# Kernel optimization log

Measured on AMD Instinct MI355X. Metric: run time of the kernel, lower is better.

## Reference

```python
import jax, jax.numpy as jnp
from jax import lax
import numpy as np

EVAL_TERMS = 10   # eval mode: num_terms = eval_terms, update_iters = 0
INIT_ITERS = 50   # power iterations done in __init__
KSIZE = 3
IDX = np.array([0, 1, 1, 2, 3, 4, 2, 4, 3])  # maps 5 coeffs -> 3x3 kernel
EPS = 1e-12


def _l2n(t, axis):
    return t / (jnp.sqrt(jnp.sum(t * t, axis=axis, keepdims=True)) + EPS)


def setup_inputs() -> dict:
    key = jax.random.key(0)
    kx, kw, kb, ku, kv = jax.random.split(key, 5)
    C = 64
    stdv = 1.0 / np.sqrt(C)
    return {
        "x": jax.random.normal(kx, (16, C, 192, 192), dtype=jnp.float32),
        "random_conv_filter": jax.random.normal(kw, (C, C, 5), dtype=jnp.float32) * stdv,
        "bias": jax.random.uniform(kb, (C,), dtype=jnp.float32, minval=-stdv, maxval=stdv),
        "u0": jax.random.normal(ku, (5, 1, C), dtype=jnp.float32),
        "v0": jax.random.normal(kv, (5, C, 1), dtype=jnp.float32),
    }


def _power_iter(A, u0, v0):
    # A: (num, C, C) (stop-gradient), u: (num,1,C), v: (num,C,1)
    u = _l2n(u0, 2)
    v = _l2n(v0, 1)
    def body(i, uv):
        u, v = uv
        v = _l2n(jnp.sum(A * u, axis=2, keepdims=True), 1)
        u = _l2n(jnp.sum(A * v, axis=1, keepdims=True), 2)
        return (u, v)
    return lax.fori_loop(0, INIT_ITERS, body, (u, v))


def reference(x, random_conv_filter, bias, u0, v0):
    C = random_conv_filter.shape[0]
    # skew-symmetric filter per coefficient slice: A = 0.5*(W - W^T)
    A = 0.5 * (random_conv_filter - jnp.transpose(random_conv_filter, (1, 0, 2)))
    A = jnp.transpose(A, (2, 0, 1))  # (num, C, C)
    # spectral norm via power iteration (buffers; no grad)
    u, v = _power_iter(lax.stop_gradient(A), u0, v0)
    u = lax.stop_gradient(u)
    v = lax.stop_gradient(v)
    sigmas = jnp.sum(A * v * u, axis=(1, 2))  # (num,), grad flows through A only
    An = A / sigmas[:, None, None]
    # Taylor series of expm: I + An + An^2/2! + ... (eval_terms=10)
    curr = An
    Fm = An
    for i in range(2, EVAL_TERMS + 1):
        curr = jnp.einsum('nij,njk->nik', curr, An) / float(i)
        Fm = Fm + curr
    Fm = Fm + jnp.eye(C, dtype=Fm.dtype)[None]
    Fm = jnp.transpose(Fm, (1, 2, 0))  # (C, C, num)
    # expand 5 coeffs to 3x3 kernel, then spatial ifft2 -> real
    K = Fm[:, :, IDX].reshape(C, C, KSIZE, KSIZE)
    K = jnp.fft.ifft2(K, axes=(-2, -1)).real.astype(x.dtype)
    w = x.shape[2]
    pad = w // KSIZE  # circular pad and matching dilation
    xp = jnp.pad(x, ((0, 0), (0, 0), (pad, pad), (pad, pad)), mode='wrap')
    z = lax.conv_general_dilated(
        xp, K, window_strides=(1, 1), padding='VALID',
        rhs_dilation=(pad, pad),
        dimension_numbers=('NCHW', 'OIHW', 'NCHW'))
    return z + bias[None, :, None, None]
```

## Files before the change

### kernel.cpp

```cpp
#include <hip/hip_runtime.h>

typedef __attribute__((ext_vector_type(8))) short short8;
typedef __attribute__((ext_vector_type(4))) float f32x4;
typedef __attribute__((ext_vector_type(4))) float float4v;
typedef __attribute__((ext_vector_type(4))) unsigned int u32x4;

__device__ __forceinline__ unsigned short f2bf(float f) {
    unsigned int u = __float_as_uint(f);
    u += 0x7fffu + ((u >> 16) & 1u);
    return (unsigned short)(u >> 16);
}

__device__ __forceinline__ float wavesum(float x) {
#pragma unroll
    for (int m = 1; m < 64; m <<= 1) x += __shfl_xor(x, m);
    return x;
}

__device__ __forceinline__ float wavemax(float x) {
#pragma unroll
    for (int m = 1; m < 64; m <<= 1) x = fmaxf(x, __shfl_xor(x, m));
    return x;
}

__device__ __forceinline__ float matvec64(const float* row, float y) {
    float ac[8] = {0.f, 0.f, 0.f, 0.f, 0.f, 0.f, 0.f, 0.f};
#pragma unroll
    for (int j = 0; j < 64; ++j) {
        const float yj =
            __uint_as_float(__builtin_amdgcn_readlane(__float_as_uint(y), j));
        ac[j & 7] = fmaf(row[j], yj, ac[j & 7]);
    }
    return ((ac[0] + ac[1]) + (ac[2] + ac[3])) + ((ac[4] + ac[5]) + (ac[6] + ac[7]));
}

__device__ __forceinline__ void gload16(const void* g, void* l) {
    __builtin_amdgcn_global_load_lds(
        (const __attribute__((address_space(1))) unsigned int*)g,
        (__attribute__((address_space(3))) unsigned int*)l, 16, 0, 0);
}

#define WTF_OFF       81920
#define WTOLD_OFF     745472
#define XT_OFF        1441792
#define WS_NEEDED     76939264UL

#define FM_AFP   0
#define FM_R0    17408
#define FM_R1    34816
#define FM_SLOT  52224
#define FM_RED   76800
#define FM_SMEM  76928

__device__ __forceinline__ void fm_matmul_sb(char* sm, int srcOff, int bfSrcSlot,
                                             int dstOff, int bfDstSlot, int t) {
    const float* src = (const float*)(sm + srcOff);
    const unsigned short* bfS =
        (const unsigned short*)(sm + FM_SLOT) + bfSrcSlot * 4096;
    float* dst = (float*)(sm + dstOff);
    float* redf = (float*)(sm + FM_RED);
    const int lane = t & 63;
    const int wv = t >> 6;
    const int lm = lane & 15, lg = lane >> 4;
    f32x4 acc[4] = {};
    if (t < 256) {
#pragma unroll
        for (int kk = 0; kk < 2; ++kk) {
            const float* ap = src + (16 * wv + lm) * 68 + kk * 32 + lg * 8;
            const f32x4 a0 = *(const f32x4*)ap;
            const f32x4 a1 = *(const f32x4*)(ap + 4);
            short8 ah;
#pragma unroll
            for (int j = 0; j < 4; ++j) {
                ah[j] = (short)f2bf(a0[j]);
                ah[j + 4] = (short)f2bf(a1[j]);
            }
#pragma unroll
            for (int cf = 0; cf < 4; ++cf) {
                const short8 b =
                    *(const short8*)(bfS + ((kk * 4 + cf) * 64 + lane) * 8);
                acc[cf] = __builtin_amdgcn_mfma_f32_16x16x32_bf16(ah, b, acc[cf],
                                                                  0, 0, 0);
            }
        }
        float mx = 0.0f;
#pragma unroll
        for (int cf = 0; cf < 4; ++cf)
#pragma unroll
            for (int r = 0; r < 4; ++r) mx = fmaxf(mx, fabsf(acc[cf][r]));
        mx = wavemax(mx);
        if (lane == 0) redf[wv] = mx;
    }
    __syncthreads();
    if (t < 256) {
        const float g = fmaxf(fmaxf(redf[0], redf[1]), fmaxf(redf[2], redf[3]));
        const float sc = 1.0f / g;
        unsigned short* bfD = (unsigned short*)(sm + FM_SLOT) + bfDstSlot * 4096;
#pragma unroll
        for (int cf = 0; cf < 4; ++cf) {
#pragma unroll
            for (int r = 0; r < 4; ++r) {
                const int k = 16 * wv + 4 * lg + r;
                const int nn = 16 * cf + lm;
                const float v = acc[cf][r] * sc;
                dst[k * 68 + nn] = v;
                if (bfDstSlot >= 0)
                    bfD[(((k >> 5) * 4 + cf) * 64 + ((k & 31) >> 3) * 16 + lm) * 8 +
                        (k & 7)] = f2bf(v);
            }
        }
    }
    __syncthreads();
}

__global__ __launch_bounds__(512) void fmconv_kernel(const float* __restrict__ W,
                                                     const float* __restrict__ u0,
                                                     const float* __restrict__ x,
                                                     float* __restrict__ FmOut,
                                                     unsigned short* __restrict__ xT) {
    __shared__ __align__(16) char smem[FM_SMEM];
    const int t = threadIdx.x;

    if (blockIdx.x >= 5) {
        float (*L0)[66] = (float (*)[66])smem;
        float (*L1)[66] = (float (*)[66])(smem + 8448);
        const int bb = blockIdx.x - 5;
        const int n = bb / 96;
        const int hpair = bb % 96;
        const int c = t >> 4;
        const int w4 = (t & 15) * 4;
        const int w2 = t >> 3;
        const int c4 = (t & 7) * 4;

#define XADDR(I)                                                                \
    (x + ((size_t)((n * 64 + ((I) & 1) * 32 + c) * 192 +                        \
                   (hpair * 2 + (I) / 6))) * 192 + (((I) >> 1) % 3) * 64 + w4)

        float4v r = *(const float4v*)XADDR(0);
        float4v rn;
#pragma unroll
        for (int i = 0; i < 12; ++i) {
            float (*L)[66] = (i & 1) ? L1 : L0;
            if (i < 11) rn = *(const float4v*)XADDR(i + 1);
            L[c][w4 + 0] = r[0];
            L[c][w4 + 1] = r[1];
            L[c][w4 + 2] = r[2];
            L[c][w4 + 3] = r[3];
            __syncthreads();
            union { unsigned short u[4]; unsigned long long q; } pk;
#pragma unroll
            for (int k = 0; k < 4; ++k) pk.u[k] = f2bf(L[c4 + k][w2]);
            const int half = i & 1;
            const int wb = (i >> 1) % 3;
            const int dh = i / 6;
            const size_t tilebase =
                ((size_t)(((n * 192 + hpair * 2 + dh) * 2 + half))) * 6144 + wb * 2048;
            *(unsigned long long*)(xT + tilebase + w2 * 32 + c4) = pk.q;
            r = rn;
        }
#undef XADDR
        return;
    }

    float* Afp = (float*)(smem + FM_AFP);
    float* R0f = (float*)(smem + FM_R0);
    float* R1f = (float*)(smem + FM_R1);
    float* redf = (float*)(smem + FM_RED);
    float* sigP = redf + 4;
    const int n = blockIdx.x;
    const int lane = t & 63;
    const int wv = t >> 6;
    const int lm = lane & 15, lg = lane >> 4;

    {
        const int i = t >> 3;
        const int j0 = (t & 7) * 8;
#pragma unroll
        for (int k = 0; k < 8; ++k) {
            const int j = j0 + k;
            const float wij = W[(i * 64 + j) * 5 + n];
            const float wji = W[(j * 64 + i) * 5 + n];
            Afp[i * 68 + j] = 0.5f * (wij - wji);
        }
    }
    __syncthreads();

    if (t < 256) {
        unsigned short* s0 = (unsigned short*)(smem + FM_SLOT);
#pragma unroll
        for (int cf = 0; cf < 4; ++cf) {
#pragma unroll
            for (int r = 0; r < 4; ++r) {
                const int k = 16 * wv + 4 * lg + r;
                const int nn = 16 * cf + lm;
                s0[(((k >> 5) * 4 + cf) * 64 + ((k & 31) >> 3) * 16 + lm) * 8 +
                   (k & 7)] = f2bf(Afp[k * 68 + nn]);
            }
        }
    }
    __syncthreads();

    fm_matmul_sb(smem, FM_AFP, 0, FM_R0, 1, t);
    fm_matmul_sb(smem, FM_R0, 1, FM_R1, 2, t);
    fm_matmul_sb(smem, FM_R1, 2, FM_R0, 0, t);
    fm_matmul_sb(smem, FM_R0, 0, FM_R1, 2, t);
    fm_matmul_sb(smem, FM_R1, 2, FM_R0, 0, t);
    fm_matmul_sb(smem, FM_R0, 0, FM_R1, -1, t);
    fm_matmul_sb(smem, FM_R1, 0, FM_R0, -1, t);
    fm_matmul_sb(smem, FM_R0, 1, FM_R1, -1, t);

    if (t < 64) {
        float row[64];
#pragma unroll
        for (int q = 0; q < 16; ++q)
            *(f32x4*)&row[q * 4] = *(const f32x4*)&R1f[t * 68 + q * 4];
        float u = u0[n * 64 + t];
        u = u / (sqrtf(wavesum(u * u)) + 1e-12f);
        const float w = matvec64(row, u);
#pragma unroll
        for (int q = 0; q < 16; ++q)
            *(f32x4*)&row[q * 4] = *(const f32x4*)&Afp[t * 68 + q * 4];
        const float tt = matvec64(row, w);
        const float v = tt / (sqrtf(wavesum(tt * tt)) + 1e-12f);
        const float s = matvec64(row, v);
        const float u50 = -s / (sqrtf(wavesum(s * s)) + 1e-12f);
        const float t2 = matvec64(row, u50);
        const float sig = wavesum(v * t2);
        if (t == 0) *sigP = sig;
    }
    __syncthreads();

    const float inv_sig = 1.0f / (*sigP);
    float Fm[4][4];
    if (t < 256) {
        unsigned int* Anpk = (unsigned int*)(smem + FM_SLOT);
#pragma unroll
        for (int cf = 0; cf < 4; ++cf) {
#pragma unroll
            for (int r = 0; r < 4; ++r) {
                const int k = 16 * wv + 4 * lg + r;
                const int nn = 16 * cf + lm;
                const float v = Afp[k * 68 + nn] * inv_sig;
                R0f[k * 68 + nn] = v;
                const unsigned int ph = f2bf(v);
                const float hf = __uint_as_float(ph << 16);
                const unsigned int pl = f2bf(v - hf);
                Anpk[(((k >> 5) * 4 + cf) * 64 + ((k & 31) >> 3) * 16 + lm) * 8 +
                     (k & 7)] = ph | (pl << 16);
                Fm[cf][r] = v;
            }
        }
    }
    __syncthreads();

    for (int term = 2; term <= 10; ++term) {
        f32x4 acc[4] = {};
        if (t < 256) {
            const unsigned int* Anpk = (const unsigned int*)(smem + FM_SLOT);
#pragma unroll
            for (int kk = 0; kk < 2; ++kk) {
                const float* ap = R0f + (16 * wv + lm) * 68 + kk * 32 + lg * 8;
                const f32x4 a0 = *(const f32x4*)ap;
                const f32x4 a1 = *(const f32x4*)(ap + 4);
                short8 ah, al;
#pragma unroll
                for (int j = 0; j < 4; ++j) {
                    const unsigned int h0 = f2bf(a0[j]);
                    ah[j] = (short)h0;
                    al[j] = (short)f2bf(a0[j] - __uint_as_float(h0 << 16));
                    const unsigned int h1 = f2bf(a1[j]);
                    ah[j + 4] = (short)h1;
                    al[j + 4] = (short)f2bf(a1[j] - __uint_as_float(h1 << 16));
                }
#pragma unroll
                for (int cf = 0; cf < 4; ++cf) {
                    const unsigned int* pp = Anpk + ((kk * 4 + cf) * 64 + lane) * 8;
                    const u32x4 p0 = *(const u32x4*)pp;
                    const u32x4 p1 = *(const u32x4*)(pp + 4);
                    short8 bh, bl;
#pragma unroll
                    for (int j = 0; j < 4; ++j) {
                        bh[j] = (short)(p0[j] & 0xffffu);
                        bl[j] = (short)(p0[j] >> 16);
                        bh[j + 4] = (short)(p1[j] & 0xffffu);
                        bl[j + 4] = (short)(p1[j] >> 16);
                    }
                    acc[cf] = __builtin_amdgcn_mfma_f32_16x16x32_bf16(ah, bh,
                                                                      acc[cf], 0, 0, 0);
                    acc[cf] = __builtin_amdgcn_mfma_f32_16x16x32_bf16(ah, bl,
                                                                      acc[cf], 0, 0, 0);
                    acc[cf] = __builtin_amdgcn_mfma_f32_16x16x32_bf16(al, bh,
                                                                      acc[cf], 0, 0, 0);
                }
            }
        }
        __syncthreads();
        if (t < 256) {
            const float sc = 1.0f / (float)term;
#pragma unroll
            for (int cf = 0; cf < 4; ++cf) {
#pragma unroll
                for (int r = 0; r < 4; ++r) {
                    const int k = 16 * wv + 4 * lg + r;
                    const int nn = 16 * cf + lm;
                    const float v = acc[cf][r] * sc;
                    Fm[cf][r] += v;
                    if (term < 10) R0f[k * 68 + nn] = v;
                }
            }
        }
        __syncthreads();
    }

    if (t < 256) {
#pragma unroll
        for (int cf = 0; cf < 4; ++cf) {
#pragma unroll
            for (int r = 0; r < 4; ++r) {
                const int k = 16 * wv + 4 * lg + r;
                const int nn = 16 * cf + lm;
                FmOut[n * 4096 + k * 64 + nn] = Fm[cf][r] + ((k == nn) ? 1.0f : 0.0f);
            }
        }
    }
}

__global__ __launch_bounds__(256) void wbuild_kernel(const float* __restrict__ Fm,
                                                     unsigned short* __restrict__ Wtf,
                                                     unsigned short* __restrict__ WtOld) {
    const int tg = blockIdx.x * 256 + threadIdx.x;
    const int o = tg >> 6;
    const int i = tg & 63;
    float f[5];
#pragma unroll
    for (int nn = 0; nn < 5; ++nn) f[nn] = Fm[nn * 4096 + o * 64 + i];
    const int idx[3][3] = {{0, 1, 1}, {2, 3, 4}, {2, 4, 3}};
    float Kk[3][3];
#pragma unroll
    for (int u = 0; u < 3; ++u) {
#pragma unroll
        for (int v = 0; v < 3; ++v) {
            float s = 0.0f;
#pragma unroll
            for (int p = 0; p < 3; ++p) {
#pragma unroll
                for (int q = 0; q < 3; ++q) {
                    const int m = (p * u + q * v) % 3;
                    s += f[idx[p][q]] * ((m == 0) ? 1.0f : -0.5f);
                }
            }
            Kk[u][v] = s * (1.0f / 9.0f);
        }
    }
#pragma unroll
    for (int a = 0; a < 3; ++a) {
#pragma unroll
        for (int b = 0; b < 3; ++b) {
            const int m = (a * 3 + b) * 64 + o;
#pragma unroll
            for (int al = 0; al < 3; ++al) {
#pragma unroll
                for (int be = 0; be < 3; ++be) {
                    const int kh = (al - a + 4) % 3;
                    const int kw = (be - b + 4) % 3;
                    const unsigned short bf = f2bf(Kk[kh][kw]);
                    const int kap = (al * 3 + be) * 64 + i;
                    WtOld[m * 576 + kap] = bf;
                    const int MF = m >> 4, lmx = m & 15;
                    const int cc = kap >> 5, lgx = (kap >> 3) & 3, j = kap & 7;
                    Wtf[MF * 9216 + cc * 512 + (lgx * 16 + lmx) * 8 + j] = bf;
                }
            }
        }
    }
}

__global__ __launch_bounds__(256, 2) void gemm4_kernel(
    const unsigned short* __restrict__ xT, const unsigned short* __restrict__ Wtf,
    const float* __restrict__ bias, float* __restrict__ out) {
    __shared__ __align__(16) char smem[81920];
    const int t = threadIdx.x;
    const int lane = t & 63;
    const int wv = t >> 6;
    const int wm = wv >> 1;
    const int wp = wv & 1;
    const int lm = lane & 15;
    const int lg = lane >> 4;

    const int orig = blockIdx.x;
    const int swz = (orig & 7) * 192 + (orig >> 3);
    const int mg = swz % 3;
    const int panel = swz / 3;
    const int n = panel >> 5;
    const int h0b = (panel & 31) * 2;

    f32x4 acc[6][4] = {};

#define STAGE(BUF, KC)                                                          \
    {                                                                           \
        const int al_ = (KC) / 3, be_ = (KC) - 3 * ((KC) / 3);                  \
        _Pragma("unroll") for (int it = 0; it < 10; ++it) {                     \
            char* ldsb = smem + (BUF) * 40960 + it * 4096 + wv * 1024;          \
            const unsigned short* src;                                          \
            if (it < 6) {                                                       \
                const int e = it * 2048 + t * 8;                                \
                const int mfL = e >> 10;                                        \
                const int rem = e & 1023;                                       \
                src = Wtf + (mg * 12 + mfL) * 9216 + (KC) * 1024 + rem;         \
            } else {                                                            \
                const int e = (it - 6) * 2048 + t * 8;                          \
                const int ccL = e >> 12;                                        \
                const int rem = e & 4095;                                       \
                const int p_ = rem >> 5;                                        \
                const int c_ = rem & 31;                                        \
                const int h_ = h0b + (p_ >> 6) + 64 * al_;                      \
                const int w_ = be_ * 64 + (p_ & 63);                            \
                src = xT + ((size_t)((n * 192 + h_) * 2 + ccL)) * 6144 +        \
                      w_ * 32 + c_;                                             \
            }                                                                   \
            gload16(src, ldsb);                                                 \
        }                                                                       \
    }

#define COMPUTE(BUF)                                                            \
    {                                                                           \
        const char* base = smem + (BUF) * 40960;                                \
        short8 af[12];                                                          \
        short8 bf[8];                                                           \
        _Pragma("unroll") for (int mf = 0; mf < 6; ++mf)                        \
            _Pragma("unroll") for (int cl = 0; cl < 2; ++cl)                    \
                af[mf * 2 + cl] = *(const short8*)(                             \
                    base + (wm * 6 + mf) * 2048 + cl * 1024 + lane * 16);       \
        _Pragma("unroll") for (int pf = 0; pf < 4; ++pf)                        \
            _Pragma("unroll") for (int cl = 0; cl < 2; ++cl)                    \
                bf[pf * 2 + cl] = *(const short8*)(                             \
                    base + 24576 + cl * 8192 +                                  \
                    (wp * 64 + pf * 16 + lm) * 64 + lg * 16);                   \
        _Pragma("unroll") for (int cl = 0; cl < 2; ++cl)                        \
            _Pragma("unroll") for (int mf = 0; mf < 6; ++mf)                    \
                _Pragma("unroll") for (int pf = 0; pf < 4; ++pf)                \
                    acc[mf][pf] = __builtin_amdgcn_mfma_f32_16x16x32_bf16(      \
                        af[mf * 2 + cl], bf[pf * 2 + cl], acc[mf][pf], 0, 0, 0);\
    }

    STAGE(0, 0);
    __syncthreads();
#pragma unroll
    for (int kc = 0; kc < 9; ++kc) {
        const int b = kc & 1;
        if (kc < 8) STAGE(b ^ 1, kc + 1);
        COMPUTE(b);
        if (kc < 8) __syncthreads();
    }
#undef STAGE
#undef COMPUTE

    const int h0 = h0b + wp;
#pragma unroll
    for (int mf = 0; mf < 6; ++mf) {
#pragma unroll
        for (int r = 0; r < 4; ++r) {
            const int m = mg * 192 + wm * 96 + mf * 16 + lg * 4 + r;
            const int o = m & 63;
            const int ab2 = m >> 6;
            const float bo = bias[o];
            const int rowoff =
                ((n * 64 + o) * 192 + (h0 + 64 * (ab2 / 3))) * 192 + 64 * (ab2 % 3);
#pragma unroll
            for (int pf = 0; pf < 4; ++pf) {
                out[rowoff + pf * 16 + lm] = acc[mf][pf][r] + bo;
            }
        }
    }
}

__global__ __launch_bounds__(256) void gemm_fallback(const float* __restrict__ x,
                                                     const unsigned short* __restrict__ Wt,
                                                     const float* __restrict__ bias,
                                                     float* __restrict__ out) {
    __shared__ unsigned short Xs[64][36];
    const int t = threadIdx.x;
    const int lane = t & 63;
    const int wv = t >> 6;
    const int pblk = blockIdx.x;
    const int mg = blockIdx.y;
    const int n = pblk >> 6;
    const int h0 = pblk & 63;
    const int wave_m0 = mg * 192 + wv * 48;
    const int lm = lane & 15;
    const int lg = lane >> 4;

    f32x4 acc[3][4] = {};
    const float* xb = x + n * 64 * 36864;
    const int w0s = t & 63;
    const int kq = (t >> 6) * 8;

    for (int c = 0; c < 18; ++c) {
        const int ab = c >> 1;
        const int al = ab / 3;
        const int be = ab % 3;
        const int ih = (c & 1) * 32;
        const int base = ih * 36864 + (h0 + 64 * al) * 192 + 64 * be + w0s;
#pragma unroll
        for (int s = 0; s < 8; ++s) {
            const int kp = kq + s;
            Xs[w0s][kp] = f2bf(xb[base + kp * 36864]);
        }
        __syncthreads();
        const int kb = c * 32 + lg * 8;
        short8 af[3];
#pragma unroll
        for (int mf = 0; mf < 3; ++mf)
            af[mf] = *(const short8*)(Wt + (wave_m0 + mf * 16 + lm) * 576 + kb);
        short8 bf[4];
#pragma unroll
        for (int pf = 0; pf < 4; ++pf) {
            union { short8 v; unsigned long long q[2]; } u;
            const unsigned long long* s8 =
                (const unsigned long long*)(&Xs[pf * 16 + lm][lg * 8]);
            u.q[0] = s8[0];
            u.q[1] = s8[1];
            bf[pf] = u.v;
        }
#pragma unroll
        for (int mf = 0; mf < 3; ++mf)
#pragma unroll
            for (int pf = 0; pf < 4; ++pf)
                acc[mf][pf] = __builtin_amdgcn_mfma_f32_16x16x32_bf16(
                    af[mf], bf[pf], acc[mf][pf], 0, 0, 0);
        __syncthreads();
    }

#pragma unroll
    for (int mf = 0; mf < 3; ++mf)
#pragma unroll
        for (int r = 0; r < 4; ++r) {
            const int m = wave_m0 + mf * 16 + lg * 4 + r;
            const int o = m & 63;
            const int ab2 = m >> 6;
            const float bo = bias[o];
            const int rowoff =
                ((n * 64 + o) * 192 + (h0 + 64 * (ab2 / 3))) * 192 + 64 * (ab2 % 3);
#pragma unroll
            for (int pf = 0; pf < 4; ++pf)
                out[rowoff + pf * 16 + lm] = acc[mf][pf][r] + bo;
        }
}

extern "C" void kernel_launch(void* const* d_in, const int* in_sizes, int n_in,
                              void* d_out, int out_size, void* d_ws, size_t ws_size,
                              hipStream_t stream) {
    (void)in_sizes; (void)n_in; (void)out_size;
    const float* x = (const float*)d_in[0];
    const float* W = (const float*)d_in[1];
    const float* bias = (const float*)d_in[2];
    const float* u0 = (const float*)d_in[3];
    float* out = (float*)d_out;

    float* Fm = (float*)d_ws;
    unsigned short* Wtf = (unsigned short*)((char*)d_ws + WTF_OFF);
    unsigned short* WtOld = (unsigned short*)((char*)d_ws + WTOLD_OFF);
    unsigned short* xT = (unsigned short*)((char*)d_ws + XT_OFF);

    const bool big_ws = (ws_size >= WS_NEEDED);

    if (big_ws) {
        fmconv_kernel<<<5 + 1536, 512, 0, stream>>>(W, u0, x, Fm, xT);
        wbuild_kernel<<<16, 256, 0, stream>>>(Fm, Wtf, WtOld);
        gemm4_kernel<<<1536, 256, 0, stream>>>(xT, Wtf, bias, out);
    } else {
        fmconv_kernel<<<5, 512, 0, stream>>>(W, u0, x, Fm, xT);
        wbuild_kernel<<<16, 256, 0, stream>>>(Fm, Wtf, WtOld);
        dim3 g(1024, 3, 1);
        gemm_fallback<<<g, 256, 0, stream>>>(x, WtOld, bias, out);
    }
}
```

Baseline: 112.8 us.

## Fuse x bf16 conversion into GEMM B-tile staging, drop xT pre-pass

Removes the separate pass that transposed x into a bf16 xT workspace buffer. The GEMM kernel now loads fp32 x into registers, converts it to bf16 and writes the B tile to LDS itself, with register prefetch overlapping the MFMA compute. This saves the extra global write and re-read of the intermediate tensor. In exchange the GEMM carries more registers, and its uncoalesced fp32 loads (stride across channels) plus the LDS stores sit on its critical path.

```diff
diff --git a/kernel.cpp b/kernel.cpp
--- a/kernel.cpp
+++ b/kernel.cpp
@@ -42,8 +42,7 @@
 
 #define WTF_OFF       81920
 #define WTOLD_OFF     745472
-#define XT_OFF        1441792
-#define WS_NEEDED     76939264UL
+#define WS_NEEDED     1409024UL
 
 #define FM_AFP   0
 #define FM_R0    17408
@@ -113,55 +112,11 @@
     __syncthreads();
 }
 
-__global__ __launch_bounds__(512) void fmconv_kernel(const float* __restrict__ W,
-                                                     const float* __restrict__ u0,
-                                                     const float* __restrict__ x,
-                                                     float* __restrict__ FmOut,
-                                                     unsigned short* __restrict__ xT) {
+__global__ __launch_bounds__(512) void fm_kernel(const float* __restrict__ W,
+                                                 const float* __restrict__ u0,
+                                                 float* __restrict__ FmOut) {
     __shared__ __align__(16) char smem[FM_SMEM];
     const int t = threadIdx.x;
-
-    if (blockIdx.x >= 5) {
-        float (*L0)[66] = (float (*)[66])smem;
-        float (*L1)[66] = (float (*)[66])(smem + 8448);
-        const int bb = blockIdx.x - 5;
-        const int n = bb / 96;
-        const int hpair = bb % 96;
-        const int c = t >> 4;
-        const int w4 = (t & 15) * 4;
-        const int w2 = t >> 3;
-        const int c4 = (t & 7) * 4;
-
-#define XADDR(I)                                                                \
-    (x + ((size_t)((n * 64 + ((I) & 1) * 32 + c) * 192 +                        \
-                   (hpair * 2 + (I) / 6))) * 192 + (((I) >> 1) % 3) * 64 + w4)
-
-        float4v r = *(const float4v*)XADDR(0);
-        float4v rn;
-#pragma unroll
-        for (int i = 0; i < 12; ++i) {
-            float (*L)[66] = (i & 1) ? L1 : L0;
-            if (i < 11) rn = *(const float4v*)XADDR(i + 1);
-            L[c][w4 + 0] = r[0];
-            L[c][w4 + 1] = r[1];
-            L[c][w4 + 2] = r[2];
-            L[c][w4 + 3] = r[3];
-            __syncthreads();
-            union { unsigned short u[4]; unsigned long long q; } pk;
-#pragma unroll
-            for (int k = 0; k < 4; ++k) pk.u[k] = f2bf(L[c4 + k][w2]);
-            const int half = i & 1;
-            const int wb = (i >> 1) % 3;
-            const int dh = i / 6;
-            const size_t tilebase =
-                ((size_t)(((n * 192 + hpair * 2 + dh) * 2 + half))) * 6144 + wb * 2048;
-            *(unsigned long long*)(xT + tilebase + w2 * 32 + c4) = pk.q;
-            r = rn;
-        }
-#undef XADDR
-        return;
-    }
-
     float* Afp = (float*)(smem + FM_AFP);
     float* R0f = (float*)(smem + FM_R0);
     float* R1f = (float*)(smem + FM_R1);
@@ -375,8 +330,8 @@
     }
 }
 
-__global__ __launch_bounds__(256, 2) void gemm4_kernel(
-    const unsigned short* __restrict__ xT, const unsigned short* __restrict__ Wtf,
+__global__ __launch_bounds__(256, 2) void gemm5_kernel(
+    const float* __restrict__ x, const unsigned short* __restrict__ Wtf,
     const float* __restrict__ bias, float* __restrict__ out) {
     __shared__ __align__(16) char smem[81920];
     const int t = threadIdx.x;
@@ -395,30 +350,39 @@
     const int h0b = (panel & 31) * 2;
 
     f32x4 acc[6][4] = {};
-
-#define STAGE(BUF, KC)                                                          \
+    float R[4][8];
+
+    const float* xb = x + (size_t)n * 2359296 + lane;
+
+#define ASTAGE(BUF, KC)                                                         \
+    {                                                                           \
+        _Pragma("unroll") for (int it = 0; it < 6; ++it) {                      \
+            char* ldsb = smem + (BUF) * 40960 + it * 4096 + wv * 1024;          \
+            const int e = it * 2048 + t * 8;                                    \
+            const int mfL = e >> 10;                                            \
+            const int rem = e & 1023;                                           \
+            gload16(Wtf + (mg * 12 + mfL) * 9216 + (KC) * 1024 + rem, ldsb);    \
+        }                                                                       \
+    }
+
+#define BLOAD(KC)                                                               \
     {                                                                           \
         const int al_ = (KC) / 3, be_ = (KC) - 3 * ((KC) / 3);                  \
-        _Pragma("unroll") for (int it = 0; it < 10; ++it) {                     \
-            char* ldsb = smem + (BUF) * 40960 + it * 4096 + wv * 1024;          \
-            const unsigned short* src;                                          \
-            if (it < 6) {                                                       \
-                const int e = it * 2048 + t * 8;                                \
-                const int mfL = e >> 10;                                        \
-                const int rem = e & 1023;                                       \
-                src = Wtf + (mg * 12 + mfL) * 9216 + (KC) * 1024 + rem;         \
-            } else {                                                            \
-                const int e = (it - 6) * 2048 + t * 8;                          \
-                const int ccL = e >> 12;                                        \
-                const int rem = e & 4095;                                       \
-                const int p_ = rem >> 5;                                        \
-                const int c_ = rem & 31;                                        \
-                const int h_ = h0b + (p_ >> 6) + 64 * al_;                      \
-                const int w_ = be_ * 64 + (p_ & 63);                            \
-                src = xT + ((size_t)((n * 192 + h_) * 2 + ccL)) * 6144 +        \
-                      w_ * 32 + c_;                                             \
-            }                                                                   \
-            gload16(src, ldsb);                                                 \
+        const float* xc = xb + (h0b + 64 * al_) * 192 + be_ * 64;               \
+        _Pragma("unroll") for (int j = 0; j < 4; ++j)                           \
+            _Pragma("unroll") for (int k = 0; k < 8; ++k)                       \
+                R[j][k] = xc[(size_t)((j >> 1) * 32 + wv * 8 + k) * 36864 +     \
+                             (j & 1) * 192];                                    \
+    }
+
+#define BSTORE(BUF)                                                             \
+    {                                                                           \
+        _Pragma("unroll") for (int j = 0; j < 4; ++j) {                         \
+            union { unsigned short us[8]; short8 v; } pk;                       \
+            _Pragma("unroll") for (int k = 0; k < 8; ++k)                       \
+                pk.us[k] = f2bf(R[j][k]);                                       \
+            *(short8*)(smem + (BUF) * 40960 + 24576 + (j >> 1) * 8192 +         \
+                       ((j & 1) * 64 + lane) * 64 + wv * 16) = pk.v;            \
         }                                                                       \
     }
 
@@ -443,16 +407,24 @@
                         af[mf * 2 + cl], bf[pf * 2 + cl], acc[mf][pf], 0, 0, 0);\
     }
 
-    STAGE(0, 0);
+    BLOAD(0);
+    ASTAGE(0, 0);
+    BSTORE(0);
     __syncthreads();
 #pragma unroll
     for (int kc = 0; kc < 9; ++kc) {
         const int b = kc & 1;
-        if (kc < 8) STAGE(b ^ 1, kc + 1);
+        if (kc < 8) {
+            BLOAD(kc + 1);
+            ASTAGE(b ^ 1, kc + 1);
+        }
         COMPUTE(b);
-        if (kc < 8) __syncthreads();
-    }
-#undef STAGE
+        if (kc < 8) BSTORE(b ^ 1);
+        __syncthreads();
+    }
+#undef ASTAGE
+#undef BLOAD
+#undef BSTORE
 #undef COMPUTE
 
     const int h0 = h0b + wp;
@@ -560,17 +532,13 @@
     float* Fm = (float*)d_ws;
     unsigned short* Wtf = (unsigned short*)((char*)d_ws + WTF_OFF);
     unsigned short* WtOld = (unsigned short*)((char*)d_ws + WTOLD_OFF);
-    unsigned short* xT = (unsigned short*)((char*)d_ws + XT_OFF);
-
-    const bool big_ws = (ws_size >= WS_NEEDED);
-
-    if (big_ws) {
-        fmconv_kernel<<<5 + 1536, 512, 0, stream>>>(W, u0, x, Fm, xT);
-        wbuild_kernel<<<16, 256, 0, stream>>>(Fm, Wtf, WtOld);
-        gemm4_kernel<<<1536, 256, 0, stream>>>(xT, Wtf, bias, out);
+
+    fm_kernel<<<5, 512, 0, stream>>>(W, u0, Fm);
+    wbuild_kernel<<<16, 256, 0, stream>>>(Fm, Wtf, WtOld);
+
+    if (ws_size >= WS_NEEDED) {
+        gemm5_kernel<<<1536, 256, 0, stream>>>(x, Wtf, bias, out);
     } else {
-        fmconv_kernel<<<5, 512, 0, stream>>>(W, u0, x, Fm, xT);
-        wbuild_kernel<<<16, 256, 0, stream>>>(Fm, Wtf, WtOld);
         dim3 g(1024, 3, 1);
         gemm_fallback<<<g, 256, 0, stream>>>(x, WtOld, bias, out);
     }
```

Result: slower. 129.2 us (+14.6%).
